# Optimization experiments

Measured on AMD Instinct MI355X. Metric: run time of the kernel, lower is better.

## Reference

```python
import jax, jax.numpy as jnp
import numpy as np

N = 50000   # nodes
E = 800000  # edges (avg degree 16)
D = 128     # dim_node_features
G = 128     # num_graphs
NP = 25000  # post nodes
NI = 25000  # image nodes
L = 2       # num_gnn_layers
EPS = 1e-5


def setup_inputs() -> dict:
    key = jax.random.key(0)
    ks = jax.random.split(key, 24)
    f = lambda k, shp, s: jax.random.normal(k, shp, jnp.float32) * s
    inp = {
        "x": f(ks[0], (N, D), 1.0),
        "W_gnn": f(ks[1], (L, D, D), D ** -0.5),
        "b_gnn": f(ks[2], (L, D), 0.02),
        "hbn_gamma": 1.0 + f(ks[3], (D,), 0.02),
        "hbn_beta": f(ks[4], (D,), 0.02),
        "gf_w1": f(ks[5], (4 * D, D), (4 * D) ** -0.5),
        "gf_b1": f(ks[6], (D,), 0.02),
        "gf_w2": f(ks[7], (D, D), D ** -0.5),
        "gf_b2": f(ks[8], (D,), 0.02),
        "bn2_gamma": 1.0 + f(ks[9], (D,), 0.02),
        "bn2_beta": f(ks[10], (D,), 0.02),
        "fl_w1": f(ks[11], (D, 64), D ** -0.5),
        "fl_b1": f(ks[12], (64,), 0.02),
        "fl_w2": f(ks[13], (64, 32), 64 ** -0.5),
        "fl_b2": f(ks[14], (32,), 0.02),
        "out_w": f(ks[15], (32, 2), 32 ** -0.5),
        "out_b": f(ks[16], (2,), 0.02),
        "edge_index": jax.random.randint(ks[17], (2, E), 0, N, jnp.int32),
        "post_idx": jax.random.randint(ks[18], (NP,), 0, N, jnp.int32),
        "image_idx": jax.random.randint(ks[19], (NI,), 0, N, jnp.int32),
        "batch_vec": jnp.sort(jax.random.randint(ks[20], (N,), 0, G, jnp.int32)),
    }
    return inp


def _bn(x, gamma, beta):
    # BatchNorm1d, training mode: biased batch statistics
    m = jnp.mean(x, axis=0)
    v = jnp.var(x, axis=0)
    return (x - m) * jax.lax.rsqrt(v + EPS) * gamma + beta


def _mean_pool(feat, seg):
    s = jax.ops.segment_sum(feat, seg, num_segments=G)
    c = jax.ops.segment_sum(jnp.ones(seg.shape[0], feat.dtype), seg, num_segments=G)
    return s / jnp.clip(c, 1.0)[:, None]


def reference(x, W_gnn, b_gnn, hbn_gamma, hbn_beta, gf_w1, gf_b1, gf_w2, gf_b2,
              bn2_gamma, bn2_beta, fl_w1, fl_b1, fl_w2, fl_b2, out_w, out_b,
              edge_index, post_idx, image_idx, batch_vec):
    src, dst = edge_index[0], edge_index[1]
    # GCN symmetric normalization with self loops: deg includes the self loop
    deg = jax.ops.segment_sum(jnp.ones(E, x.dtype), dst, num_segments=N) + 1.0
    dis = deg ** -0.5  # deg^-1/2
    enorm = (dis[src] * dis[dst])[:, None]   # per-edge norm
    snorm = (dis * dis)[:, None]             # self-loop norm
    H = x
    for i in range(L):
        xw = H @ W_gnn[i]                                   # [N, D]
        agg = jax.ops.segment_sum(xw[src] * enorm, dst, num_segments=N)
        H = agg + xw * snorm + b_gnn[i]
        H = jax.nn.leaky_relu(H)
    H = _bn(H, hbn_gamma, hbn_beta)
    pf = _mean_pool(H[post_idx], batch_vec[post_idx])        # [G, D]
    imf = _mean_pool(H[image_idx], batch_vec[image_idx])     # [G, D]
    comb = jnp.concatenate([pf, imf, pf - imf, pf * imf], axis=-1)  # [G, 4D]
    # generate_feature (dropout = identity, eval)
    h = jax.nn.leaky_relu(comb @ gf_w1 + gf_b1) @ gf_w2 + gf_b2
    h = _bn(h, bn2_gamma, bn2_beta)
    # feature_layer (encodeMLP)
    out = jax.nn.leaky_relu(h @ fl_w1 + fl_b1) @ fl_w2 + fl_b2  # [G, 32]
    prob = out @ out_w + out_b                                   # [G, 2]
    return out, prob
```

## Files before the change

### kernel.cpp

```cpp
#include <hip/hip_runtime.h>
#include <hip/hip_bf16.h>
#include <math.h>

#define DF 128
#define PSPLIT 4
#define CHUNK 8192
#define NBK 256
#define LEAKY(x) ((x) > 0.f ? (x) : 0.01f * (x))

typedef __attribute__((ext_vector_type(8))) short short8v;
typedef __attribute__((ext_vector_type(4))) float f32x4;
typedef __attribute__((ext_vector_type(4))) unsigned short u16x4;
typedef __attribute__((ext_vector_type(8))) unsigned short u16x8;

static __device__ __forceinline__ unsigned short f2bf(float f) {
  unsigned u = __float_as_uint(f);
  unsigned r = u + 0x7fffu + ((u >> 16) & 1u);
  return (unsigned short)(r >> 16);
}
static __device__ __forceinline__ float bf2f(unsigned short b) {
  return __uint_as_float(((unsigned)b) << 16);
}

__global__ void fused_pre_k(const int* __restrict__ dst, int* __restrict__ degc,
                            int* __restrict__ bhist,
                            const int* __restrict__ post_idx, const int* __restrict__ image_idx,
                            const int* __restrict__ batch, int* __restrict__ pcnt,
                            int* __restrict__ icnt,
                            const float* __restrict__ W, unsigned short* __restrict__ Wb,
                            int nE, int NP, int NI, int wTotal, int EB, int PB) {
  int b = blockIdx.x;
  if (b < EB) {
    __shared__ int lh[NBK];
    for (int i = threadIdx.x; i < NBK; i += 256) lh[i] = 0;
    __syncthreads();
    for (int i = b * 256 + threadIdx.x; i < nE; i += EB * 256) {
      int d = dst[i];
      atomicAdd(&degc[d], 1);
      atomicAdd(&lh[d >> 8], 1);
    }
    __syncthreads();
    for (int i = threadIdx.x; i < NBK; i += 256)
      if (lh[i]) atomicAdd(&bhist[i], lh[i]);
  } else if (b < EB + PB) {
    int i = (b - EB) * 256 + threadIdx.x;
    if (i < NP) atomicAdd(&pcnt[batch[post_idx[i]]], 1);
    else if (i < NP + NI) atomicAdd(&icnt[batch[image_idx[i - NP]]], 1);
  } else {
    int i = (b - EB - PB) * 256 + threadIdx.x;
    if (i < wTotal) {
      int layer = i >> 14, o = i & 16383;
      int j = o & 7, l = (o >> 3) & 63, ks = (o >> 9) & 3, ct = (o >> 11) & 3, wc = (o >> 13) & 1;
      int row = ks * 32 + (l >> 4) * 8 + j;
      int col = wc * 64 + ct * 16 + (l & 15);
      Wb[i] = f2bf(W[((size_t)layer << 14) + row * DF + col]);
    }
  }
}

__global__ void blk_sum_k(const int* __restrict__ cnt, int* __restrict__ bsum, int n) {
  __shared__ int sh[1024];
  int idx = blockIdx.x * 1024 + threadIdx.x;
  sh[threadIdx.x] = (idx < n) ? cnt[idx] : 0;
  __syncthreads();
  for (int ofs = 512; ofs > 0; ofs >>= 1) {
    if (threadIdx.x < (unsigned)ofs) sh[threadIdx.x] += sh[threadIdx.x + ofs];
    __syncthreads();
  }
  if (threadIdx.x == 0) bsum[blockIdx.x] = sh[0];
}

__global__ void __launch_bounds__(1024) scan4_k(
    const int* __restrict__ bsum, int* __restrict__ boff, int NB,
    const int* __restrict__ bhist, int* __restrict__ boff2, int* __restrict__ bcur, int NBUCK,
    const int* __restrict__ pcnt, int* __restrict__ poff, int* __restrict__ pcur,
    const int* __restrict__ icnt, int* __restrict__ ioff, int* __restrict__ icur, int G) {
  const int* in; int* out; int* cur; int n;
  if (blockIdx.x == 0)      { in = bsum;  out = boff;  cur = nullptr; n = NB; }
  else if (blockIdx.x == 1) { in = bhist; out = boff2; cur = bcur;    n = NBUCK; }
  else if (blockIdx.x == 2) { in = pcnt;  out = poff;  cur = pcur;    n = G; }
  else                      { in = icnt;  out = ioff;  cur = icur;    n = G; }
  __shared__ int sh[1024];
  int v = (threadIdx.x < (unsigned)n) ? in[threadIdx.x] : 0;
  sh[threadIdx.x] = v;
  __syncthreads();
  for (int ofs = 1; ofs < 1024; ofs <<= 1) {
    int t = (threadIdx.x >= (unsigned)ofs) ? sh[threadIdx.x - ofs] : 0;
    __syncthreads();
    sh[threadIdx.x] += t;
    __syncthreads();
  }
  if (threadIdx.x < (unsigned)n) {
    int ex = sh[threadIdx.x] - v;
    out[threadIdx.x] = ex;
    if (cur) cur[threadIdx.x] = ex;
  }
  if (threadIdx.x == 0) out[n] = sh[1023];
}

__global__ void blk_scan_dis_k(const int* __restrict__ cnt, const int* __restrict__ boff,
                               int* __restrict__ rowoff, int* __restrict__ cursor,
                               float* __restrict__ dis, int n) {
  __shared__ int sh[1024];
  int idx = blockIdx.x * 1024 + threadIdx.x;
  int v = (idx < n) ? cnt[idx] : 0;
  sh[threadIdx.x] = v;
  __syncthreads();
  for (int ofs = 1; ofs < 1024; ofs <<= 1) {
    int t = (threadIdx.x >= (unsigned)ofs) ? sh[threadIdx.x - ofs] : 0;
    __syncthreads();
    sh[threadIdx.x] += t;
    __syncthreads();
  }
  if (idx < n) {
    int ex = boff[blockIdx.x] + sh[threadIdx.x] - v;
    rowoff[idx] = ex; cursor[idx] = ex;
    dis[idx] = 1.0f / sqrtf((float)v + 1.0f);
    if (idx == n - 1) rowoff[n] = ex + v;
  }
}

__global__ void __launch_bounds__(256) bucket_fill_k(const int* __restrict__ src,
                                                     const int* __restrict__ dst,
                                                     int* __restrict__ bcur,
                                                     int* __restrict__ ebuck, int nE) {
  __shared__ int hist[NBK];
  __shared__ int base[NBK];
  __shared__ int gbase[NBK];
  __shared__ int lpack[CHUNK];
  __shared__ unsigned char lbk[CHUNK];
  int e0 = blockIdx.x * CHUNK;
  int cnt = nE - e0; if (cnt > CHUNK) cnt = CHUNK;
  for (int i = threadIdx.x; i < NBK; i += 256) hist[i] = 0;
  __syncthreads();
  for (int i = threadIdx.x; i < cnt; i += 256)
    atomicAdd(&hist[dst[e0 + i] >> 8], 1);
  __syncthreads();
  int t = threadIdx.x;
  base[t] = hist[t];
  __syncthreads();
  for (int ofs = 1; ofs < NBK; ofs <<= 1) {
    int tv = (t >= ofs) ? base[t - ofs] : 0;
    __syncthreads();
    base[t] += tv;
    __syncthreads();
  }
  int excl = base[t] - hist[t];
  __syncthreads();
  base[t] = excl;
  hist[t] = 0;
  __syncthreads();
  for (int i = threadIdx.x; i < cnt; i += 256) {
    int d = dst[e0 + i], s = src[e0 + i];
    int bk = d >> 8;
    int pos = base[bk] + atomicAdd(&hist[bk], 1);
    lpack[pos] = (s << 8) | (d & 255);
    lbk[pos] = (unsigned char)bk;
  }
  __syncthreads();
  int c = hist[t];
  gbase[t] = c > 0 ? atomicAdd(&bcur[t], c) : 0;
  __syncthreads();
  for (int i = threadIdx.x; i < cnt; i += 256) {
    int bk = lbk[i];
    ebuck[gbase[bk] + (i - base[bk])] = lpack[i];
  }
}

__global__ void __launch_bounds__(512) csr_fine_k(const int* __restrict__ boff2,
                                                  const int* __restrict__ ebuck,
                                                  const float* __restrict__ dis,
                                                  int* __restrict__ cursor,
                                                  int2* __restrict__ epack) {
  int b = blockIdx.x;
  int beg = boff2[b], end = boff2[b + 1];
  int node0 = b << 8;
  for (int i = beg + threadIdx.x; i < end; i += 512) {
    int v = ebuck[i];
    int s = v >> 8, d = node0 + (v & 255);
    int p = atomicAdd(&cursor[d], 1);
    int2 w; w.x = s; w.y = __float_as_int(dis[s] * dis[d]);
    epack[p] = w;
  }
}

__global__ void pool_fill_k(const int* __restrict__ post_idx, const int* __restrict__ image_idx,
                            const int* __restrict__ batch, int* __restrict__ pcur,
                            int* __restrict__ icur, int* __restrict__ plist,
                            int* __restrict__ ilist, int NP, int NI) {
  int i = blockIdx.x * 256 + threadIdx.x;
  if (i < NP) {
    int nd = post_idx[i];
    int p = atomicAdd(&pcur[batch[nd]], 1);
    plist[p] = nd;
  } else if (i < NP + NI) {
    int nd = image_idx[i - NP];
    int p = atomicAdd(&icur[batch[nd]], 1);
    ilist[p] = nd;
  }
}

template<bool BF16A>
__global__ void __launch_bounds__(256) gemm_mfma_k(const float* __restrict__ A,
                                                   const unsigned short* __restrict__ Ab,
                                                   const unsigned short* __restrict__ Wb,
                                                   unsigned short* __restrict__ xwb, int n) {
  const int w = threadIdx.x >> 6, l = threadIdx.x & 63;
  const int wr = w & 1, wc = w >> 1;
  const int r0 = blockIdx.x * 32 + wr * 16;
  const int row = r0 + (l & 15);
  const int kg = l >> 4;
  short8v bf[4][4];
  const unsigned short* wp = Wb + (size_t)wc * 8192 + (size_t)l * 8;
#pragma unroll
  for (int ct = 0; ct < 4; ++ct)
#pragma unroll
    for (int ks = 0; ks < 4; ++ks)
      bf[ct][ks] = *(const short8v*)(wp + ((ct * 4 + ks) << 9));
  const bool rok = row < n;
  short8v af[4];
  if constexpr (BF16A) {
    const unsigned short* ap = Ab + (size_t)row * DF + kg * 8;
#pragma unroll
    for (int ks = 0; ks < 4; ++ks)
      af[ks] = rok ? *(const short8v*)(ap + ks * 32) : (short8v)0;
  } else {
    const float* ap = A + (size_t)row * DF + kg * 8;
#pragma unroll
    for (int ks = 0; ks < 4; ++ks) {
      if (rok) {
        float4 lo = *(const float4*)(ap + ks * 32);
        float4 hi = *(const float4*)(ap + ks * 32 + 4);
        short8v t;
        t[0] = (short)f2bf(lo.x); t[1] = (short)f2bf(lo.y);
        t[2] = (short)f2bf(lo.z); t[3] = (short)f2bf(lo.w);
        t[4] = (short)f2bf(hi.x); t[5] = (short)f2bf(hi.y);
        t[6] = (short)f2bf(hi.z); t[7] = (short)f2bf(hi.w);
        af[ks] = t;
      } else af[ks] = (short8v)0;
    }
  }
  f32x4 acc[4];
#pragma unroll
  for (int ct = 0; ct < 4; ++ct) acc[ct] = (f32x4)(0.f);
#pragma unroll
  for (int ks = 0; ks < 4; ++ks)
#pragma unroll
    for (int ct = 0; ct < 4; ++ct)
      acc[ct] = __builtin_amdgcn_mfma_f32_16x16x32_bf16(af[ks], bf[ct][ks], acc[ct], 0, 0, 0);
#pragma unroll
  for (int ct = 0; ct < 4; ++ct) {
    int c = wc * 64 + ct * 16 + (l & 15);
#pragma unroll
    for (int rg = 0; rg < 4; ++rg) {
      int r = r0 + kg * 4 + rg;
      if (r < n) xwb[(size_t)r * DF + c] = f2bf(acc[ct][rg]);
    }
  }
}

__global__ void gather_k(const unsigned short* __restrict__ xwb, const int* __restrict__ rowoff,
                         const int2* __restrict__ epack, const float* __restrict__ dis,
                         const float* __restrict__ b, unsigned short* __restrict__ Hb, int n) {
  int gid = blockIdx.x * 256 + threadIdx.x;
  int node = gid >> 5;
  if (node >= n) return;
  int part = gid & 15;
  int team = (gid >> 4) & 1;
  int beg = rowoff[node], end = rowoff[node + 1];
  float acc[8];
#pragma unroll
  for (int j = 0; j < 8; ++j) acc[j] = 0.f;
  int p = beg + team;
  for (; p + 6 < end; p += 8) {
    int2 q0 = epack[p], q1 = epack[p + 2], q2 = epack[p + 4], q3 = epack[p + 6];
    float e0 = __int_as_float(q0.y), e1 = __int_as_float(q1.y);
    float e2 = __int_as_float(q2.y), e3 = __int_as_float(q3.y);
    u16x8 v0 = *(const u16x8*)(xwb + (size_t)q0.x * DF + part * 8);
    u16x8 v1 = *(const u16x8*)(xwb + (size_t)q1.x * DF + part * 8);
    u16x8 v2 = *(const u16x8*)(xwb + (size_t)q2.x * DF + part * 8);
    u16x8 v3 = *(const u16x8*)(xwb + (size_t)q3.x * DF + part * 8);
#pragma unroll
    for (int j = 0; j < 8; ++j) {
      acc[j] = fmaf(bf2f(v0[j]), e0, acc[j]);
      acc[j] = fmaf(bf2f(v1[j]), e1, acc[j]);
      acc[j] = fmaf(bf2f(v2[j]), e2, acc[j]);
      acc[j] = fmaf(bf2f(v3[j]), e3, acc[j]);
    }
  }
  for (; p < end; p += 2) {
    int2 q = epack[p];
    float e = __int_as_float(q.y);
    u16x8 v = *(const u16x8*)(xwb + (size_t)q.x * DF + part * 8);
#pragma unroll
    for (int j = 0; j < 8; ++j) acc[j] = fmaf(bf2f(v[j]), e, acc[j]);
  }
#pragma unroll
  for (int j = 0; j < 8; ++j) acc[j] += __shfl_down(acc[j], 16, 32);
  if (team == 0) {
    float dd = dis[node], sn = dd * dd;
    u16x8 xv = *(const u16x8*)(xwb + (size_t)node * DF + part * 8);
    const float* bp = b + part * 8;
    u16x8 o;
#pragma unroll
    for (int j = 0; j < 8; ++j) {
      float r = fmaf(bf2f(xv[j]), sn, acc[j]) + bp[j];
      r = LEAKY(r);
      o[j] = f2bf(r);
    }
    *(u16x8*)(Hb + (size_t)node * DF + part * 8) = o;
  }
}

__global__ void post_k(const unsigned short* __restrict__ Hb,
                       const int* __restrict__ goff_p, const int* __restrict__ mlist_p,
                       const int* __restrict__ goff_i, const int* __restrict__ mlist_i,
                       float* __restrict__ psum, float* __restrict__ isum,
                       float* __restrict__ bns, int n, int PGB, int SB) {
  int b = blockIdx.x;
  if (b < 2 * PGB) {
    int which = b >= PGB;
    int bb = which ? b - PGB : b;
    const int* goff  = which ? goff_i  : goff_p;
    const int* mlist = which ? mlist_i : mlist_p;
    float* out       = which ? isum    : psum;
    int g = bb / PSPLIT, sub = bb % PSPLIT;
    int part = threadIdx.x & 31, slot = threadIdx.x >> 5;
    int beg = goff[g], end = goff[g + 1];
    float4 acc = make_float4(0.f, 0.f, 0.f, 0.f);
    for (int j = beg + sub * 8 + slot; j < end; j += PSPLIT * 8) {
      u16x4 v = *(const u16x4*)(Hb + (size_t)mlist[j] * DF + part * 4);
      acc.x += bf2f(v[0]); acc.y += bf2f(v[1]); acc.z += bf2f(v[2]); acc.w += bf2f(v[3]);
    }
    __shared__ float4 sh[256];
    sh[threadIdx.x] = acc;
    __syncthreads();
    for (int ofs = 128; ofs >= 32; ofs >>= 1) {
      if (threadIdx.x < (unsigned)ofs) {
        float4 o = sh[threadIdx.x + ofs];
        float4 a = sh[threadIdx.x];
        a.x += o.x; a.y += o.y; a.z += o.z; a.w += o.w;
        sh[threadIdx.x] = a;
      }
      __syncthreads();
    }
    if (threadIdx.x < 32) {
      float4 a = sh[threadIdx.x];
      float* o = out + (size_t)g * DF + part * 4;
      atomicAdd(o + 0, a.x);
      atomicAdd(o + 1, a.y);
      atomicAdd(o + 2, a.z);
      atomicAdd(o + 3, a.w);
    }
  } else {
    int sb = b - 2 * PGB;
    int c = threadIdx.x & (DF - 1);
    int half = threadIdx.x >> 7;
    float s = 0.f, q = 0.f;
    for (int r = sb * 2 + half; r < n; r += SB * 2) {
      float v = bf2f(Hb[(size_t)r * DF + c]);
      s += v; q += v * v;
    }
    __shared__ float ls[256], lq[256];
    ls[threadIdx.x] = s; lq[threadIdx.x] = q;
    __syncthreads();
    if (half == 0) {
      atomicAdd(&bns[c], ls[c] + ls[c + DF]);
      atomicAdd(&bns[DF + c], lq[c] + lq[c + DF]);
    }
  }
}

__global__ void __launch_bounds__(512) head1_k(const float* __restrict__ psum,
                        const int* __restrict__ pcnt,
                        const float* __restrict__ isum, const int* __restrict__ icnt,
                        const float* __restrict__ bns, const float* __restrict__ hbn_gamma,
                        const float* __restrict__ hbn_beta, int nN,
                        const float* __restrict__ gf_w1, const float* __restrict__ gf_b1,
                        const float* __restrict__ gf_w2, const float* __restrict__ gf_b2,
                        float* __restrict__ hbuf) {
  int g = blockIdx.x;
  int j = threadIdx.x & 127, kq = threadIdx.x >> 7;
  __shared__ float comb[4 * DF];
  __shared__ float part[512];
  __shared__ float t1[DF];
  if (kq == 0) {
    float m = bns[j] / (float)nN;
    float var = bns[DF + j] / (float)nN - m * m;
    if (var < 0.f) var = 0.f;
    float sc = hbn_gamma[j] / sqrtf(var + 1e-5f);
    float sh = hbn_beta[j] - m * sc;
    int pc = pcnt[g], ic = icnt[g];
    float pf = pc > 0 ? (psum[(size_t)g * DF + j] / (float)pc) * sc + sh : 0.f;
    float im = ic > 0 ? (isum[(size_t)g * DF + j] / (float)ic) * sc + sh : 0.f;
    comb[j] = pf;
    comb[DF + j] = im;
    comb[2 * DF + j] = pf - im;
    comb[3 * DF + j] = pf * im;
  }
  __syncthreads();
  float acc = 0.f;
  const float* w1 = gf_w1 + (size_t)kq * 128 * DF + j;
#pragma unroll 8
  for (int kk = 0; kk < 128; ++kk)
    acc = fmaf(comb[kq * 128 + kk], w1[(size_t)kk * DF], acc);
  part[threadIdx.x] = acc;
  __syncthreads();
  if (kq == 0)
    t1[j] = LEAKY(gf_b1[j] + part[j] + part[128 + j] + part[256 + j] + part[384 + j]);
  __syncthreads();
  acc = 0.f;
  const float* w2 = gf_w2 + (size_t)kq * 32 * DF + j;
#pragma unroll 8
  for (int kk = 0; kk < 32; ++kk)
    acc = fmaf(t1[kq * 32 + kk], w2[(size_t)kk * DF], acc);
  part[threadIdx.x] = acc;
  __syncthreads();
  if (kq == 0)
    hbuf[(size_t)g * DF + j] = gf_b2[j] + part[j] + part[128 + j] + part[256 + j] + part[384 + j];
}

__global__ void __launch_bounds__(1024) bn2_k(const float* __restrict__ hbuf,
                      const float* __restrict__ gamma, const float* __restrict__ beta,
                      float* __restrict__ ss2, int G) {
  int c = threadIdx.x & 127, slot = threadIdx.x >> 7;
  float s = 0.f, q = 0.f;
  for (int r = slot; r < G; r += 8) {
    float v = hbuf[(size_t)r * DF + c];
    s += v; q += v * v;
  }
  __shared__ float ls[1024], lq[1024];
  ls[threadIdx.x] = s; lq[threadIdx.x] = q;
  __syncthreads();
  for (int ofs = 512; ofs >= 128; ofs >>= 1) {
    if (threadIdx.x < (unsigned)ofs) {
      ls[threadIdx.x] += ls[threadIdx.x + ofs];
      lq[threadIdx.x] += lq[threadIdx.x + ofs];
    }
    __syncthreads();
  }
  if (threadIdx.x < 128) {
    float m = ls[c] / (float)G;
    float var = lq[c] / (float)G - m * m;
    if (var < 0.f) var = 0.f;
    float sc = gamma[c] / sqrtf(var + 1e-5f);
    ss2[c] = sc;
    ss2[DF + c] = beta[c] - m * sc;
  }
}

__global__ void __launch_bounds__(512) head2_k(const float* __restrict__ hbuf,
                        const float* __restrict__ ss2,
                        const float* __restrict__ fl_w1, const float* __restrict__ fl_b1,
                        const float* __restrict__ fl_w2, const float* __restrict__ fl_b2,
                        const float* __restrict__ out_w, const float* __restrict__ out_b,
                        float* __restrict__ d_out, int G) {
  int g = blockIdx.x, t = threadIdx.x;
  __shared__ float hb[DF], part[512], t1[64], ov[32];
  if (t < DF) hb[t] = hbuf[(size_t)g * DF + t] * ss2[t] + ss2[DF + t];
  __syncthreads();
  {
    int j = t & 63, kq = t >> 6;
    float acc = 0.f;
    const float* w = fl_w1 + (size_t)kq * 16 * 64 + j;
#pragma unroll
    for (int kk = 0; kk < 16; ++kk)
      acc = fmaf(hb[kq * 16 + kk], w[(size_t)kk * 64], acc);
    part[t] = acc;
  }
  __syncthreads();
  if (t < 64) {
    float s = fl_b1[t];
#pragma unroll
    for (int i = 0; i < 8; ++i) s += part[i * 64 + t];
    t1[t] = LEAKY(s);
  }
  __syncthreads();
  {
    int j = t & 31, kq = t >> 5;
    float acc = 0.f;
    const float* w = fl_w2 + (size_t)kq * 4 * 32 + j;
#pragma unroll
    for (int kk = 0; kk < 4; ++kk)
      acc = fmaf(t1[kq * 4 + kk], w[(size_t)kk * 32], acc);
    part[t] = acc;
  }
  __syncthreads();
  if (t < 32) {
    float s = fl_b2[t];
#pragma unroll
    for (int i = 0; i < 16; ++i) s += part[i * 32 + t];
    d_out[(size_t)g * 32 + t] = s;
    ov[t] = s;
  }
  __syncthreads();
  if (t < 64) {
    int j = t & 1, kq = t >> 1;
    part[t] = ov[kq] * out_w[(size_t)kq * 2 + j];
  }
  __syncthreads();
  if (t < 2) {
    float s = out_b[t];
#pragma unroll
    for (int i = 0; i < 32; ++i) s += part[i * 2 + t];
    d_out[(size_t)G * 32 + (size_t)g * 2 + t] = s;
  }
}

extern "C" void kernel_launch(void* const* d_in, const int* in_sizes, int n_in,
                              void* d_out, int out_size, void* d_ws, size_t ws_size,
                              hipStream_t stream) {
  const float* x         = (const float*)d_in[0];
  const float* W_gnn     = (const float*)d_in[1];
  const float* b_gnn     = (const float*)d_in[2];
  const float* hbn_gamma = (const float*)d_in[3];
  const float* hbn_beta  = (const float*)d_in[4];
  const float* gf_w1     = (const float*)d_in[5];
  const float* gf_b1     = (const float*)d_in[6];
  const float* gf_w2     = (const float*)d_in[7];
  const float* gf_b2     = (const float*)d_in[8];
  const float* bn2_gamma = (const float*)d_in[9];
  const float* bn2_beta  = (const float*)d_in[10];
  const float* fl_w1     = (const float*)d_in[11];
  const float* fl_b1     = (const float*)d_in[12];
  const float* fl_w2     = (const float*)d_in[13];
  const float* fl_b2     = (const float*)d_in[14];
  const float* out_w     = (const float*)d_in[15];
  const float* out_b     = (const float*)d_in[16];
  const int* edge_index  = (const int*)d_in[17];
  const int* post_idx    = (const int*)d_in[18];
  const int* image_idx   = (const int*)d_in[19];
  const int* batch_vec   = (const int*)d_in[20];

  const int N  = in_sizes[20];
  const int E  = in_sizes[17] / 2;
  const int NP = in_sizes[18];
  const int NI = in_sizes[19];
  const int G  = out_size / 34;
  const int L  = in_sizes[1] / (DF * DF);
  const int* src  = edge_index;
  const int* dstp = edge_index + E;
  const int NB = (N + 1023) / 1024;
  const int NBUCK = (N + 255) >> 8;
  const int EB = 256;
  const int PB = (NP + NI + 255) / 256;
  const int WT = L * DF * DF;
  const int WB = (WT + 255) / 256;
  const int PGB = G * PSPLIT;
  const int SB = 256;

  char* ws = (char*)d_ws;
  size_t off = 0;
  auto alloc = [&](size_t b) { size_t o = off; off += (b + 255) & ~(size_t)255; return o; };
  size_t zero_beg = off;
  int*   degc   = (int*)(ws + alloc((size_t)N * 4));
  int*   bhist  = (int*)(ws + alloc((size_t)NBK * 4));
  float* bns    = (float*)(ws + alloc(256 * 4));
  float* psum   = (float*)(ws + alloc((size_t)G * DF * 4));
  float* isum   = (float*)(ws + alloc((size_t)G * DF * 4));
  int*   pcnt   = (int*)(ws + alloc((size_t)G * 4));
  int*   icnt   = (int*)(ws + alloc((size_t)G * 4));
  size_t zero_bytes = off - zero_beg;
  float* dis    = (float*)(ws + alloc((size_t)N * 4));
  int*   rowoff = (int*)(ws + alloc((size_t)(N + 1) * 4));
  int*   cursor = (int*)(ws + alloc((size_t)N * 4));
  int2*  epack  = (int2*)(ws + alloc((size_t)E * 8));
  int*   ebuck  = (int*)(ws + alloc((size_t)E * 4));
  int*   boff2  = (int*)(ws + alloc((size_t)(NBK + 1) * 4));
  int*   bcur   = (int*)(ws + alloc((size_t)NBK * 4));
  int*   bsum   = (int*)(ws + alloc((size_t)(NB + 1) * 4));
  int*   boff   = (int*)(ws + alloc((size_t)(NB + 1) * 4));
  unsigned short* Wb  = (unsigned short*)(ws + alloc((size_t)WT * 2));
  unsigned short* xwb = (unsigned short*)(ws + alloc((size_t)N * DF * 2));
  unsigned short* Hb  = (unsigned short*)(ws + alloc((size_t)N * DF * 2));
  int*   poff   = (int*)(ws + alloc((size_t)(G + 1) * 4));
  int*   ioff   = (int*)(ws + alloc((size_t)(G + 1) * 4));
  int*   pcur   = (int*)(ws + alloc((size_t)G * 4));
  int*   icur   = (int*)(ws + alloc((size_t)G * 4));
  int*   plist  = (int*)(ws + alloc((size_t)NP * 4));
  int*   ilist  = (int*)(ws + alloc((size_t)NI * 4));
  float* hbuf   = (float*)(ws + alloc((size_t)G * DF * 4));
  float* ss2    = (float*)(ws + alloc(256 * 4));

  hipMemsetAsync(ws + zero_beg, 0, zero_bytes, stream);

  fused_pre_k<<<EB + PB + WB, 256, 0, stream>>>(dstp, degc, bhist, post_idx, image_idx,
                                                batch_vec, pcnt, icnt, W_gnn, Wb,
                                                E, NP, NI, WT, EB, PB);
  blk_sum_k<<<NB, 1024, 0, stream>>>(degc, bsum, N);
  scan4_k<<<4, 1024, 0, stream>>>(bsum, boff, NB, bhist, boff2, bcur, NBUCK,
                                  pcnt, poff, pcur, icnt, ioff, icur, G);
  blk_scan_dis_k<<<NB, 1024, 0, stream>>>(degc, boff, rowoff, cursor, dis, N);
  bucket_fill_k<<<(E + CHUNK - 1) / CHUNK, 256, 0, stream>>>(src, dstp, bcur, ebuck, E);
  csr_fine_k<<<NBUCK, 512, 0, stream>>>(boff2, ebuck, dis, cursor, epack);
  pool_fill_k<<<(NP + NI + 255) / 256, 256, 0, stream>>>(post_idx, image_idx, batch_vec,
                                                         pcur, icur, plist, ilist, NP, NI);

  for (int l = 0; l < L; ++l) {
    if (l == 0)
      gemm_mfma_k<false><<<(N + 31) / 32, 256, 0, stream>>>(x, nullptr,
          Wb + (size_t)l * DF * DF, xwb, N);
    else
      gemm_mfma_k<true><<<(N + 31) / 32, 256, 0, stream>>>(nullptr, Hb,
          Wb + (size_t)l * DF * DF, xwb, N);
    gather_k<<<(N * 32 + 255) / 256, 256, 0, stream>>>(xwb, rowoff, epack, dis,
                                                       b_gnn + (size_t)l * DF, Hb, N);
  }

  post_k<<<2 * PGB + SB, 256, 0, stream>>>(Hb, poff, plist, ioff, ilist,
                                           psum, isum, bns, N, PGB, SB);

  head1_k<<<G, 512, 0, stream>>>(psum, pcnt, isum, icnt, bns, hbn_gamma, hbn_beta, N,
                                 gf_w1, gf_b1, gf_w2, gf_b2, hbuf);
  bn2_k<<<1, 1024, 0, stream>>>(hbuf, bn2_gamma, bn2_beta, ss2, G);
  head2_k<<<G, 512, 0, stream>>>(hbuf, ss2, fl_w1, fl_b1, fl_w2, fl_b2, out_w, out_b,
                                 (float*)d_out, G);
}
```

Baseline: 272.8 us.

## Build CSR rows per bucket in shared memory, dropping global degree atomics and scans

Measured after the change: 237.0 us. -13.1%, faster.

```diff
diff --git a/kernel.cpp b/kernel.cpp
--- a/kernel.cpp
+++ b/kernel.cpp
@@ -22,8 +22,7 @@
   return __uint_as_float(((unsigned)b) << 16);
 }
 
-__global__ void fused_pre_k(const int* __restrict__ dst, int* __restrict__ degc,
-                            int* __restrict__ bhist,
+__global__ void fused_pre_k(const int* __restrict__ dst, int* __restrict__ bhist,
                             const int* __restrict__ post_idx, const int* __restrict__ image_idx,
                             const int* __restrict__ batch, int* __restrict__ pcnt,
                             int* __restrict__ icnt,
@@ -32,16 +31,12 @@
   int b = blockIdx.x;
   if (b < EB) {
     __shared__ int lh[NBK];
-    for (int i = threadIdx.x; i < NBK; i += 256) lh[i] = 0;
-    __syncthreads();
-    for (int i = b * 256 + threadIdx.x; i < nE; i += EB * 256) {
-      int d = dst[i];
-      atomicAdd(&degc[d], 1);
-      atomicAdd(&lh[d >> 8], 1);
-    }
-    __syncthreads();
-    for (int i = threadIdx.x; i < NBK; i += 256)
-      if (lh[i]) atomicAdd(&bhist[i], lh[i]);
+    lh[threadIdx.x] = 0;
+    __syncthreads();
+    for (int i = b * 256 + threadIdx.x; i < nE; i += EB * 256)
+      atomicAdd(&lh[dst[i] >> 8], 1);
+    __syncthreads();
+    if (lh[threadIdx.x]) atomicAdd(&bhist[threadIdx.x], lh[threadIdx.x]);
   } else if (b < EB + PB) {
     int i = (b - EB) * 256 + threadIdx.x;
     if (i < NP) atomicAdd(&pcnt[batch[post_idx[i]]], 1);
@@ -58,28 +53,14 @@
   }
 }
 
-__global__ void blk_sum_k(const int* __restrict__ cnt, int* __restrict__ bsum, int n) {
-  __shared__ int sh[1024];
-  int idx = blockIdx.x * 1024 + threadIdx.x;
-  sh[threadIdx.x] = (idx < n) ? cnt[idx] : 0;
-  __syncthreads();
-  for (int ofs = 512; ofs > 0; ofs >>= 1) {
-    if (threadIdx.x < (unsigned)ofs) sh[threadIdx.x] += sh[threadIdx.x + ofs];
-    __syncthreads();
-  }
-  if (threadIdx.x == 0) bsum[blockIdx.x] = sh[0];
-}
-
-__global__ void __launch_bounds__(1024) scan4_k(
-    const int* __restrict__ bsum, int* __restrict__ boff, int NB,
+__global__ void __launch_bounds__(1024) scan3_k(
     const int* __restrict__ bhist, int* __restrict__ boff2, int* __restrict__ bcur, int NBUCK,
     const int* __restrict__ pcnt, int* __restrict__ poff, int* __restrict__ pcur,
     const int* __restrict__ icnt, int* __restrict__ ioff, int* __restrict__ icur, int G) {
   const int* in; int* out; int* cur; int n;
-  if (blockIdx.x == 0)      { in = bsum;  out = boff;  cur = nullptr; n = NB; }
-  else if (blockIdx.x == 1) { in = bhist; out = boff2; cur = bcur;    n = NBUCK; }
-  else if (blockIdx.x == 2) { in = pcnt;  out = poff;  cur = pcur;    n = G; }
-  else                      { in = icnt;  out = ioff;  cur = icur;    n = G; }
+  if (blockIdx.x == 0)      { in = bhist; out = boff2; cur = bcur; n = NBUCK; }
+  else if (blockIdx.x == 1) { in = pcnt;  out = poff;  cur = pcur; n = G; }
+  else                      { in = icnt;  out = ioff;  cur = icur; n = G; }
   __shared__ int sh[1024];
   int v = (threadIdx.x < (unsigned)n) ? in[threadIdx.x] : 0;
   sh[threadIdx.x] = v;
@@ -93,31 +74,9 @@
   if (threadIdx.x < (unsigned)n) {
     int ex = sh[threadIdx.x] - v;
     out[threadIdx.x] = ex;
-    if (cur) cur[threadIdx.x] = ex;
+    cur[threadIdx.x] = ex;
   }
   if (threadIdx.x == 0) out[n] = sh[1023];
-}
-
-__global__ void blk_scan_dis_k(const int* __restrict__ cnt, const int* __restrict__ boff,
-                               int* __restrict__ rowoff, int* __restrict__ cursor,
-                               float* __restrict__ dis, int n) {
-  __shared__ int sh[1024];
-  int idx = blockIdx.x * 1024 + threadIdx.x;
-  int v = (idx < n) ? cnt[idx] : 0;
-  sh[threadIdx.x] = v;
-  __syncthreads();
-  for (int ofs = 1; ofs < 1024; ofs <<= 1) {
-    int t = (threadIdx.x >= (unsigned)ofs) ? sh[threadIdx.x - ofs] : 0;
-    __syncthreads();
-    sh[threadIdx.x] += t;
-    __syncthreads();
-  }
-  if (idx < n) {
-    int ex = boff[blockIdx.x] + sh[threadIdx.x] - v;
-    rowoff[idx] = ex; cursor[idx] = ex;
-    dis[idx] = 1.0f / sqrtf((float)v + 1.0f);
-    if (idx == n - 1) rowoff[n] = ex + v;
-  }
 }
 
 __global__ void __launch_bounds__(256) bucket_fill_k(const int* __restrict__ src,
@@ -131,7 +90,7 @@
   __shared__ unsigned char lbk[CHUNK];
   int e0 = blockIdx.x * CHUNK;
   int cnt = nE - e0; if (cnt > CHUNK) cnt = CHUNK;
-  for (int i = threadIdx.x; i < NBK; i += 256) hist[i] = 0;
+  hist[threadIdx.x] = 0;
   __syncthreads();
   for (int i = threadIdx.x; i < cnt; i += 256)
     atomicAdd(&hist[dst[e0 + i] >> 8], 1);
@@ -167,20 +126,57 @@
   }
 }
 
-__global__ void __launch_bounds__(512) csr_fine_k(const int* __restrict__ boff2,
-                                                  const int* __restrict__ ebuck,
-                                                  const float* __restrict__ dis,
-                                                  int* __restrict__ cursor,
-                                                  int2* __restrict__ epack) {
+__global__ void __launch_bounds__(256) csr_build_k(const int* __restrict__ boff2,
+                                                   const int* __restrict__ ebuck,
+                                                   int* __restrict__ rowoff,
+                                                   float* __restrict__ dis,
+                                                   int2* __restrict__ epack,
+                                                   int N, int NBUCK) {
   int b = blockIdx.x;
   int beg = boff2[b], end = boff2[b + 1];
   int node0 = b << 8;
-  for (int i = beg + threadIdx.x; i < end; i += 512) {
-    int v = ebuck[i];
-    int s = v >> 8, d = node0 + (v & 255);
-    int p = atomicAdd(&cursor[d], 1);
-    int2 w; w.x = s; w.y = __float_as_int(dis[s] * dis[d]);
-    epack[p] = w;
+  __shared__ int hist[NBK];
+  __shared__ int lbase[NBK];
+  int t = threadIdx.x;
+  hist[t] = 0;
+  __syncthreads();
+  for (int i = beg + t; i < end; i += 256)
+    atomicAdd(&hist[ebuck[i] & 255], 1);
+  __syncthreads();
+  int v = hist[t];
+  lbase[t] = v;
+  __syncthreads();
+  for (int ofs = 1; ofs < NBK; ofs <<= 1) {
+    int tv = (t >= ofs) ? lbase[t - ofs] : 0;
+    __syncthreads();
+    lbase[t] += tv;
+    __syncthreads();
+  }
+  int excl = lbase[t] - v;
+  __syncthreads();
+  lbase[t] = excl;
+  hist[t] = 0;
+  int node = node0 + t;
+  if (node < N) {
+    rowoff[node] = beg + excl;
+    dis[node] = 1.0f / sqrtf((float)v + 1.0f);
+  }
+  if (b == NBUCK - 1 && t == 0) rowoff[N] = end;
+  __syncthreads();
+  for (int i = beg + t; i < end; i += 256) {
+    int e = ebuck[i];
+    int loc = e & 255;
+    int pos = beg + lbase[loc] + atomicAdd(&hist[loc], 1);
+    int2 w; w.x = e >> 8; w.y = node0 + loc;
+    epack[pos] = w;
+  }
+}
+
+__global__ void enorm_k(int2* __restrict__ epack, const float* __restrict__ dis, int E) {
+  int i = blockIdx.x * 256 + threadIdx.x;
+  if (i < E) {
+    int2 w = epack[i];
+    epack[i].y = __float_as_int(dis[w.x] * dis[w.y]);
   }
 }
 
@@ -540,7 +536,6 @@
   const int L  = in_sizes[1] / (DF * DF);
   const int* src  = edge_index;
   const int* dstp = edge_index + E;
-  const int NB = (N + 1023) / 1024;
   const int NBUCK = (N + 255) >> 8;
   const int EB = 256;
   const int PB = (NP + NI + 255) / 256;
@@ -553,7 +548,6 @@
   size_t off = 0;
   auto alloc = [&](size_t b) { size_t o = off; off += (b + 255) & ~(size_t)255; return o; };
   size_t zero_beg = off;
-  int*   degc   = (int*)(ws + alloc((size_t)N * 4));
   int*   bhist  = (int*)(ws + alloc((size_t)NBK * 4));
   float* bns    = (float*)(ws + alloc(256 * 4));
   float* psum   = (float*)(ws + alloc((size_t)G * DF * 4));
@@ -563,13 +557,10 @@
   size_t zero_bytes = off - zero_beg;
   float* dis    = (float*)(ws + alloc((size_t)N * 4));
   int*   rowoff = (int*)(ws + alloc((size_t)(N + 1) * 4));
-  int*   cursor = (int*)(ws + alloc((size_t)N * 4));
   int2*  epack  = (int2*)(ws + alloc((size_t)E * 8));
   int*   ebuck  = (int*)(ws + alloc((size_t)E * 4));
   int*   boff2  = (int*)(ws + alloc((size_t)(NBK + 1) * 4));
   int*   bcur   = (int*)(ws + alloc((size_t)NBK * 4));
-  int*   bsum   = (int*)(ws + alloc((size_t)(NB + 1) * 4));
-  int*   boff   = (int*)(ws + alloc((size_t)(NB + 1) * 4));
   unsigned short* Wb  = (unsigned short*)(ws + alloc((size_t)WT * 2));
   unsigned short* xwb = (unsigned short*)(ws + alloc((size_t)N * DF * 2));
   unsigned short* Hb  = (unsigned short*)(ws + alloc((size_t)N * DF * 2));
@@ -584,15 +575,14 @@
 
   hipMemsetAsync(ws + zero_beg, 0, zero_bytes, stream);
 
-  fused_pre_k<<<EB + PB + WB, 256, 0, stream>>>(dstp, degc, bhist, post_idx, image_idx,
+  fused_pre_k<<<EB + PB + WB, 256, 0, stream>>>(dstp, bhist, post_idx, image_idx,
                                                 batch_vec, pcnt, icnt, W_gnn, Wb,
                                                 E, NP, NI, WT, EB, PB);
-  blk_sum_k<<<NB, 1024, 0, stream>>>(degc, bsum, N);
-  scan4_k<<<4, 1024, 0, stream>>>(bsum, boff, NB, bhist, boff2, bcur, NBUCK,
+  scan3_k<<<3, 1024, 0, stream>>>(bhist, boff2, bcur, NBUCK,
                                   pcnt, poff, pcur, icnt, ioff, icur, G);
-  blk_scan_dis_k<<<NB, 1024, 0, stream>>>(degc, boff, rowoff, cursor, dis, N);
   bucket_fill_k<<<(E + CHUNK - 1) / CHUNK, 256, 0, stream>>>(src, dstp, bcur, ebuck, E);
-  csr_fine_k<<<NBUCK, 512, 0, stream>>>(boff2, ebuck, dis, cursor, epack);
+  csr_build_k<<<NBUCK, 256, 0, stream>>>(boff2, ebuck, rowoff, dis, epack, N, NBUCK);
+  enorm_k<<<(E + 255) / 256, 256, 0, stream>>>(epack, dis, E);
   pool_fill_k<<<(NP + NI + 255) / 256, 256, 0, stream>>>(post_idx, image_idx, batch_vec,
                                                          pcur, icur, plist, ilist, NP, NI);
 
```
